# Kernel optimization log

Hardware: AMD Instinct MI355X
Metric: run time of the kernel (lower is better)

## Reference

```python
import jax, jax.numpy as jnp
import numpy as np

EMBED_DIM = 1024
NUM_HEADS = 16
HEAD_DIM = EMBED_DIM // NUM_HEADS
L, B, S = 2048, 2, 2048


def setup_inputs() -> dict:
    key = jax.random.key(0)
    k1, k2, k3, k4, k5, k6, k7 = jax.random.split(key, 7)
    query = jax.random.normal(k1, (L, B, EMBED_DIM), dtype=jnp.float32)
    kk = jax.random.normal(k2, (S, B, EMBED_DIM), dtype=jnp.float32)
    vv = jax.random.normal(k3, (S, B, EMBED_DIM), dtype=jnp.float32)
    # in_proj: Linear(E, 3E) -> weight (3E, E), bias (3E,)
    w_in = jax.random.normal(k4, (3 * EMBED_DIM, EMBED_DIM), dtype=jnp.float32) * (1.0 / np.sqrt(EMBED_DIM))
    b_in = jax.random.normal(k5, (3 * EMBED_DIM,), dtype=jnp.float32) * 0.02
    w_out = jax.random.normal(k6, (EMBED_DIM, EMBED_DIM), dtype=jnp.float32) * (1.0 / np.sqrt(EMBED_DIM))
    b_out = jax.random.normal(k7, (EMBED_DIM,), dtype=jnp.float32) * 0.02
    return {"query": query, "key": kk, "value": vv,
            "w_in": w_in, "b_in": b_in, "w_out": w_out, "b_out": b_out}


def _split_heads(x, seq_len, batch):
    # (T, B, E) -> (B, H, T, d)
    return x.reshape(seq_len, batch, NUM_HEADS, HEAD_DIM).transpose(1, 2, 0, 3)


def reference(query, key, value, w_in, b_in, w_out, b_out):
    seq_q, batch, _ = query.shape
    seq_kv = key.shape[0]
    # split fused in_proj into q/k/v projections (chunk along output rows)
    wq, wk, wv = jnp.split(w_in, 3, axis=0)
    bq, bk, bv = jnp.split(b_in, 3, axis=0)
    q = query @ wq.T + bq            # (L, B, E)
    k = key @ wk.T + bk              # (S, B, E)
    v = value @ wv.T + bv            # (S, B, E)
    q = _split_heads(q, seq_q, batch)   # (B, H, L, d)
    k = _split_heads(k, seq_kv, batch)  # (B, H, S, d)
    v = _split_heads(v, seq_kv, batch)  # (B, H, S, d)
    scale = jnp.asarray(np.sqrt(HEAD_DIM), dtype=q.dtype)
    scores = jnp.einsum('bhld,bhsd->bhls', q, k) / scale  # (B, H, L, S)
    attn = jax.nn.softmax(scores, axis=-1)
    context = jnp.einsum('bhls,bhsd->bhld', attn, v)      # (B, H, L, d)
    # (B, H, L, d) -> (L, B, E)
    context = context.transpose(2, 0, 1, 3).reshape(seq_q, batch, EMBED_DIM)
    attn_output = context @ w_out.T + b_out
    return attn_output
```

## Files before the change

### kernel.cpp

```cpp
#include <hip/hip_runtime.h>
#include <hip/hip_bf16.h>
#include <stdint.h>

#define L_SEQ 2048
#define S_SEQ 2048
#define BATCH 2
#define EMB 1024
#define NH 16
#define HD 64
#define MROWS 4096

typedef __bf16 bf16x8 __attribute__((ext_vector_type(8)));
typedef float f32x4 __attribute__((ext_vector_type(4)));
typedef __hip_bfloat16 bf16;

__device__ __forceinline__ f32x4 mfma16(bf16x8 a, bf16x8 b, f32x4 c) {
    return __builtin_amdgcn_mfma_f32_16x16x32_bf16(a, b, c, 0, 0, 0);
}

__device__ __forceinline__ void gll16(const bf16* g, bf16* l) {
    __builtin_amdgcn_global_load_lds(
        (const __attribute__((address_space(1))) void*)g,
        (__attribute__((address_space(3))) void*)l, 16, 0, 0);
}

__device__ __forceinline__ bf16x8 ld8_cvt(const float* p) {
    const float4 a = *reinterpret_cast<const float4*>(p);
    const float4 b = *reinterpret_cast<const float4*>(p + 4);
    union { bf16x8 v; bf16 h[8]; } u;
    u.h[0] = __float2bfloat16(a.x); u.h[1] = __float2bfloat16(a.y);
    u.h[2] = __float2bfloat16(a.z); u.h[3] = __float2bfloat16(a.w);
    u.h[4] = __float2bfloat16(b.x); u.h[5] = __float2bfloat16(b.y);
    u.h[6] = __float2bfloat16(b.z); u.h[7] = __float2bfloat16(b.w);
    return u.v;
}

__device__ __forceinline__ uint32_t packbf2(float a, float b) {
    union { bf16 h[2]; uint32_t u; } t;
    t.h[0] = __float2bfloat16(a); t.h[1] = __float2bfloat16(b);
    return t.u;
}

__global__ __launch_bounds__(256) void cvt_kernel(
    const float* __restrict__ w_in, const float* __restrict__ w_out,
    const float* __restrict__ q_in, const float* __restrict__ k_in,
    const float* __restrict__ v_in,
    bf16* __restrict__ wib, bf16* __restrict__ wob,
    bf16* __restrict__ Xq, bf16* __restrict__ Xk, bf16* __restrict__ Xv)
{
    const size_t i = ((size_t)blockIdx.x * 256 + threadIdx.x) * 8;
    const size_t o1 = (size_t)3 * EMB * EMB;
    const size_t o2 = o1 + (size_t)EMB * EMB;
    const size_t o3 = o2 + (size_t)MROWS * EMB;
    const size_t o4 = o3 + (size_t)MROWS * EMB;
    const float* src; bf16* dst; size_t j;
    if      (i < o1) { src = w_in;  dst = wib; j = i; }
    else if (i < o2) { src = w_out; dst = wob; j = i - o1; }
    else if (i < o3) { src = q_in;  dst = Xq;  j = i - o2; }
    else if (i < o4) { src = k_in;  dst = Xk;  j = i - o3; }
    else             { src = v_in;  dst = Xv;  j = i - o4; }
    *reinterpret_cast<bf16x8*>(dst + j) = ld8_cvt(src + j);
}

__global__ __launch_bounds__(256) void qkv_gemm(
    const bf16* __restrict__ Xq, const bf16* __restrict__ Xk,
    const bf16* __restrict__ Xv, const bf16* __restrict__ wib,
    const float* __restrict__ b_in,
    bf16* __restrict__ Qh, bf16* __restrict__ Kh, bf16* __restrict__ Vh)
{
    __shared__ alignas(16) bf16 lds_a[128 * 32];
    __shared__ alignas(16) bf16 lds_b[128 * 32];

    const int tid  = threadIdx.x;
    const int lane = tid & 63;
    const int wv   = tid >> 6;
    const int quad = lane >> 4;
    const int lx   = lane & 15;

    const int m0  = blockIdx.x * 128;
    const int n0g = blockIdx.y * 128;
    const int chunk = n0g >> 10;
    const bf16* Aop = (chunk == 0) ? Xq : (chunk == 1) ? Xk : Xv;

    const int wm = (wv >> 1) * 64;
    const int wn = (wv & 1) * 64;

    const int gr = 16 * wv + (lane >> 2);
    const int gc = (lane & 3) * 8;
    const bf16* gA = Aop + (size_t)(m0 + gr) * EMB + gc;
    const bf16* gB = wib + (size_t)(n0g + gr) * EMB + gc;
    bf16* lA = lds_a + wv * 512;
    bf16* lB = lds_b + wv * 512;

    f32x4 acc[4][4];
#pragma unroll
    for (int i = 0; i < 4; i++)
#pragma unroll
        for (int j = 0; j < 4; j++) acc[i][j] = (f32x4){0.f, 0.f, 0.f, 0.f};

    for (int kt = 0; kt < EMB; kt += 32) {
        __syncthreads();
        gll16(gA + kt, lA);
        gll16(gA + 64 * EMB + kt, lA + 2048);
        gll16(gB + kt, lB);
        gll16(gB + 64 * EMB + kt, lB + 2048);
        __syncthreads();

        bf16x8 af[4], bfv[4];
        const int ka = quad * 8;
#pragma unroll
        for (int sm = 0; sm < 4; sm++)
            af[sm] = *reinterpret_cast<const bf16x8*>(lds_a + (wm + sm * 16 + lx) * 32 + ka);
#pragma unroll
        for (int sn = 0; sn < 4; sn++)
            bfv[sn] = *reinterpret_cast<const bf16x8*>(lds_b + (wn + sn * 16 + lx) * 32 + ka);
#pragma unroll
        for (int sm = 0; sm < 4; sm++)
#pragma unroll
            for (int sn = 0; sn < 4; sn++)
                acc[sm][sn] = mfma16(af[sm], bfv[sn], acc[sm][sn]);
    }

    const float scale = (chunk == 0) ? 0.125f : 1.0f;
    bf16* dst = (chunk == 0) ? Qh : (chunk == 1) ? Kh : Vh;
#pragma unroll
    for (int sn = 0; sn < 4; sn++) {
        const int n_g = n0g + wn + sn * 16 + lx;
        const float bias = b_in[n_g];
        const int nc = n_g & (EMB - 1);
        const int h  = nc >> 6;
        const int dd = nc & 63;
#pragma unroll
        for (int sm = 0; sm < 4; sm++) {
#pragma unroll
            for (int r = 0; r < 4; r++) {
                const int m_g = m0 + wm + sm * 16 + quad * 4 + r;
                const int t = m_g >> 1;
                const int b = m_g & 1;
                const int bhidx = b * NH + h;
                const float v = (acc[sm][sn][r] + bias) * scale;
                dst[((size_t)bhidx * S_SEQ + t) * HD + dd] = __float2bfloat16(v);
            }
        }
    }
}

#define TST 72
__global__ __launch_bounds__(256) void transpose_v(
    const bf16* __restrict__ Vh, bf16* __restrict__ Vt)
{
    __shared__ alignas(16) bf16 t[64 * TST];
    const int tid = threadIdx.x;
    const int bh  = blockIdx.y;
    const int s0  = blockIdx.x * 64;
    const int r0  = tid >> 3;
    const int c0  = (tid & 7) * 8;

    const bf16* src = Vh + (size_t)bh * S_SEQ * HD;
    uint4 a = *reinterpret_cast<const uint4*>(src + (size_t)(s0 + r0) * HD + c0);
    uint4 b = *reinterpret_cast<const uint4*>(src + (size_t)(s0 + r0 + 32) * HD + c0);
    *reinterpret_cast<uint4*>(t + r0 * TST + c0) = a;
    *reinterpret_cast<uint4*>(t + (r0 + 32) * TST + c0) = b;
    __syncthreads();

    const int sc = (tid & 7) * 8;
    bf16* dst = Vt + (size_t)bh * HD * S_SEQ;
#pragma unroll
    for (int half = 0; half < 2; half++) {
        const int d = (tid >> 3) + half * 32;
        union { bf16 h[8]; uint4 u; } o;
#pragma unroll
        for (int j = 0; j < 8; j++) o.h[j] = t[(sc + j) * TST + d];
        *reinterpret_cast<uint4*>(dst + (size_t)d * S_SEQ + s0 + sc) = o.u;
    }
}

__global__ __launch_bounds__(512, 4) void attn_kernel(
    const bf16* __restrict__ Qh, const bf16* __restrict__ Kh,
    const bf16* __restrict__ Vt, bf16* __restrict__ ctx)
{
    __shared__ alignas(16) bf16 k_lds[128 * 64];
    __shared__ alignas(16) bf16 v_lds[64 * 128];
    __shared__ alignas(16) bf16 p_lds[8][16 * 128];

    const int tid  = threadIdx.x;
    const int lane = tid & 63;
    const int wv   = tid >> 6;
    const int quad = lane >> 4;
    const int lx   = lane & 15;
    const int lx7  = lane & 7;

    const int bh = blockIdx.y;
    const int l0 = blockIdx.x * 128;
    const int q0 = wv * 16;

    const bf16* Kbase = Kh + (size_t)bh * S_SEQ * HD;
    const bf16* Vbase = Vt + (size_t)bh * HD * S_SEQ;

    const bf16* qrow = Qh + ((size_t)bh * L_SEQ + l0 + q0 + lx) * HD + quad * 8;
    const bf16x8 qf0 = *reinterpret_cast<const bf16x8*>(qrow);
    const bf16x8 qf1 = *reinterpret_cast<const bf16x8*>(qrow + 32);

    float m_run = -1e30f, l_run = 0.f;
    f32x4 accv[4];
#pragma unroll
    for (int sn = 0; sn < 4; sn++) accv[sn] = (f32x4){0.f, 0.f, 0.f, 0.f};

    const int kr0 = tid >> 3;
    const int kc  = (tid & 7) * 8;
    const int vd0 = tid >> 4;
    const int vs  = (tid & 15) * 8;

    bf16* p_w = &p_lds[wv][0];

    for (int s0 = 0; s0 < S_SEQ; s0 += 128) {
        uint4 ka = *reinterpret_cast<const uint4*>(Kbase + (size_t)(s0 + kr0) * HD + kc);
        uint4 kb = *reinterpret_cast<const uint4*>(Kbase + (size_t)(s0 + kr0 + 64) * HD + kc);
        uint4 va = *reinterpret_cast<const uint4*>(Vbase + (size_t)vd0 * S_SEQ + s0 + vs);
        uint4 vb = *reinterpret_cast<const uint4*>(Vbase + (size_t)(vd0 + 32) * S_SEQ + s0 + vs);
        __syncthreads();
        {
            const int ksw = (((kc >> 3) ^ (kr0 & 7)) << 3);
            *reinterpret_cast<uint4*>(k_lds + kr0 * 64 + ksw) = ka;
            *reinterpret_cast<uint4*>(k_lds + (kr0 + 64) * 64 + ksw) = kb;
            const int vsw = (((vs >> 3) ^ (vd0 & 7)) << 3);
            *reinterpret_cast<uint4*>(v_lds + vd0 * 128 + vsw) = va;
            *reinterpret_cast<uint4*>(v_lds + (vd0 + 32) * 128 + vsw) = vb;
        }
        __syncthreads();

        f32x4 sc[8];
#pragma unroll
        for (int c = 0; c < 8; c++) {
            const bf16* kr = k_lds + (c * 16 + lx) * 64;
            bf16x8 kf0 = *reinterpret_cast<const bf16x8*>(kr + ((quad ^ lx7) << 3));
            bf16x8 kf1 = *reinterpret_cast<const bf16x8*>(kr + (((quad + 4) ^ lx7) << 3));
            f32x4 tt = (f32x4){0.f, 0.f, 0.f, 0.f};
            tt = mfma16(kf0, qf0, tt);
            tt = mfma16(kf1, qf1, tt);
            sc[c] = tt;
        }

        float mloc = sc[0][0];
#pragma unroll
        for (int c = 0; c < 8; c++)
#pragma unroll
            for (int r = 0; r < 4; r++) mloc = fmaxf(mloc, sc[c][r]);
        mloc = fmaxf(mloc, __shfl_xor(mloc, 16));
        mloc = fmaxf(mloc, __shfl_xor(mloc, 32));
        const float mnew = fmaxf(m_run, mloc);
        const float al = __expf(m_run - mnew);
        m_run = mnew;
        float rsum = 0.f;
#pragma unroll
        for (int c = 0; c < 8; c++)
#pragma unroll
            for (int r = 0; r < 4; r++) {
                const float p = __expf(sc[c][r] - mnew);
                sc[c][r] = p;
                rsum += p;
            }
        rsum += __shfl_xor(rsum, 16);
        rsum += __shfl_xor(rsum, 32);
        l_run = l_run * al + rsum;

#pragma unroll
        for (int r = 0; r < 4; r++) {
            const float ar = __shfl(al, quad * 20 + r);
#pragma unroll
            for (int sn = 0; sn < 4; sn++) accv[sn][r] *= ar;
        }

#pragma unroll
        for (int c = 0; c < 8; c++) {
            uint2 pk;
            pk.x = packbf2(sc[c][0], sc[c][1]);
            pk.y = packbf2(sc[c][2], sc[c][3]);
            const int off = lx * 128 + ((((c * 2 + (quad >> 1)) ^ lx7)) << 3) + ((quad & 1) << 2);
            *reinterpret_cast<uint2*>(p_w + off) = pk;
        }

#pragma unroll
        for (int sk = 0; sk < 4; sk++) {
            bf16x8 pf = *reinterpret_cast<const bf16x8*>(
                p_w + lx * 128 + ((((sk * 4 + quad) ^ lx7)) << 3));
#pragma unroll
            for (int sn = 0; sn < 4; sn++) {
                const bf16* vr = v_lds + (sn * 16 + lx) * 128 + ((((sk * 4 + quad) ^ lx7)) << 3);
                accv[sn] = mfma16(pf, *reinterpret_cast<const bf16x8*>(vr), accv[sn]);
            }
        }
    }

    const int b = bh >> 4;
    const int h = bh & 15;
#pragma unroll
    for (int r = 0; r < 4; r++) {
        const float lr = __shfl(l_run, quad * 20 + r);
        const float inv = 1.f / lr;
        const int l = l0 + q0 + quad * 4 + r;
#pragma unroll
        for (int sn = 0; sn < 4; sn++) {
            const int dd = sn * 16 + lx;
            ctx[(size_t)(l * BATCH + b) * EMB + h * HD + dd] =
                __float2bfloat16(accv[sn][r] * inv);
        }
    }
}

__global__ __launch_bounds__(256) void out_gemm(
    const bf16* __restrict__ ctx, const bf16* __restrict__ wob,
    const float* __restrict__ b_out, float* __restrict__ out)
{
    __shared__ alignas(16) bf16 lds_a[128 * 32];
    __shared__ alignas(16) bf16 lds_b[128 * 32];

    const int tid  = threadIdx.x;
    const int lane = tid & 63;
    const int wv   = tid >> 6;
    const int quad = lane >> 4;
    const int lx   = lane & 15;

    const int m0 = blockIdx.x * 128;
    const int n0 = blockIdx.y * 128;

    const int wm = (wv >> 1) * 64;
    const int wn = (wv & 1) * 64;

    const int gr = 16 * wv + (lane >> 2);
    const int gc = (lane & 3) * 8;
    const bf16* gA = ctx + (size_t)(m0 + gr) * EMB + gc;
    const bf16* gB = wob + (size_t)(n0 + gr) * EMB + gc;
    bf16* lA = lds_a + wv * 512;
    bf16* lB = lds_b + wv * 512;

    f32x4 acc[4][4];
#pragma unroll
    for (int i = 0; i < 4; i++)
#pragma unroll
        for (int j = 0; j < 4; j++) acc[i][j] = (f32x4){0.f, 0.f, 0.f, 0.f};

    for (int kt = 0; kt < EMB; kt += 32) {
        __syncthreads();
        gll16(gA + kt, lA);
        gll16(gA + 64 * EMB + kt, lA + 2048);
        gll16(gB + kt, lB);
        gll16(gB + 64 * EMB + kt, lB + 2048);
        __syncthreads();

        bf16x8 af[4], bfv[4];
        const int ka = quad * 8;
#pragma unroll
        for (int sm = 0; sm < 4; sm++)
            af[sm] = *reinterpret_cast<const bf16x8*>(lds_a + (wm + sm * 16 + lx) * 32 + ka);
#pragma unroll
        for (int sn = 0; sn < 4; sn++)
            bfv[sn] = *reinterpret_cast<const bf16x8*>(lds_b + (wn + sn * 16 + lx) * 32 + ka);
#pragma unroll
        for (int sm = 0; sm < 4; sm++)
#pragma unroll
            for (int sn = 0; sn < 4; sn++)
                acc[sm][sn] = mfma16(af[sm], bfv[sn], acc[sm][sn]);
    }

#pragma unroll
    for (int sn = 0; sn < 4; sn++) {
        const int n_g = n0 + wn + sn * 16 + lx;
        const float bias = b_out[n_g];
#pragma unroll
        for (int sm = 0; sm < 4; sm++) {
#pragma unroll
            for (int r = 0; r < 4; r++) {
                const int m_g = m0 + wm + sm * 16 + quad * 4 + r;
                out[(size_t)m_g * EMB + n_g] = acc[sm][sn][r] + bias;
            }
        }
    }
}

extern "C" void kernel_launch(void* const* d_in, const int* in_sizes, int n_in,
                              void* d_out, int out_size, void* d_ws, size_t ws_size,
                              hipStream_t stream)
{
    const float* query = (const float*)d_in[0];
    const float* key_  = (const float*)d_in[1];
    const float* value = (const float*)d_in[2];
    const float* w_in  = (const float*)d_in[3];
    const float* b_in  = (const float*)d_in[4];
    const float* w_out = (const float*)d_in[5];
    const float* b_out = (const float*)d_in[6];
    float* out = (float*)d_out;

    const size_t seg = (size_t)MROWS * EMB;
    bf16* wib = (bf16*)d_ws;
    bf16* wob = wib + (size_t)3 * EMB * EMB;
    bf16* Xq  = wob + (size_t)EMB * EMB;
    bf16* Xk  = Xq + seg;
    bf16* Xv  = Xk + seg;
    bf16* Qh  = Xv + seg;
    bf16* Kh  = Qh + seg;
    bf16* Vh  = Kh + seg;
    bf16* Vt  = Xq;
    bf16* ctx = Vh;

    cvt_kernel<<<8192, 256, 0, stream>>>(w_in, w_out, query, key_, value,
                                         wib, wob, Xq, Xk, Xv);
    qkv_gemm<<<dim3(32, 24), 256, 0, stream>>>(Xq, Xk, Xv, wib, b_in, Qh, Kh, Vh);
    transpose_v<<<dim3(32, 32), 256, 0, stream>>>(Vh, Vt);
    attn_kernel<<<dim3(16, 32), 512, 0, stream>>>(Qh, Kh, Vt, ctx);
    out_gemm<<<dim3(32, 8), 256, 0, stream>>>(ctx, wob, b_out, out);
}
```

Measured before the change: 239.5 us.

## Prefetch K/V tiles, use exp2 softmax, cheaper bf16 pack, smaller out_gemm tiles

Several independent changes. The attention loop now loads the next K/V tile into registers while the current tile is being computed, so global latency overlaps with the MFMA and softmax work. The Q scale folds in log2(e) so softmax can use the hardware exp2 directly. The bf16 pack is done with integer rounding plus a byte permute. Finally, out_gemm's M tile is halved to 64 so twice as many blocks cover the GPU. The bit-trick rounding ignores NaN handling and round-to-even ties, and the prefetch wraps around to reload the first tile on the last iteration.

```diff
diff --git a/kernel.cpp b/kernel.cpp
--- a/kernel.cpp
+++ b/kernel.cpp
@@ -36,9 +36,9 @@
 }
 
 __device__ __forceinline__ uint32_t packbf2(float a, float b) {
-    union { bf16 h[2]; uint32_t u; } t;
-    t.h[0] = __float2bfloat16(a); t.h[1] = __float2bfloat16(b);
-    return t.u;
+    const uint32_t ra = __float_as_uint(a) + 0x8000u;
+    const uint32_t rb = __float_as_uint(b) + 0x8000u;
+    return __builtin_amdgcn_perm(rb, ra, 0x07060302u);
 }
 
 __global__ __launch_bounds__(256) void cvt_kernel(
@@ -121,7 +121,7 @@
                 acc[sm][sn] = mfma16(af[sm], bfv[sn], acc[sm][sn]);
     }
 
-    const float scale = (chunk == 0) ? 0.125f : 1.0f;
+    const float scale = (chunk == 0) ? 0.18033688011112042f : 1.0f;
     bf16* dst = (chunk == 0) ? Qh : (chunk == 1) ? Kh : Vh;
 #pragma unroll
     for (int sn = 0; sn < 4; sn++) {
@@ -210,24 +210,29 @@
     const int kc  = (tid & 7) * 8;
     const int vd0 = tid >> 4;
     const int vs  = (tid & 15) * 8;
+    const int ksw = (((kc >> 3) ^ (kr0 & 7)) << 3);
+    const int vsw = (((vs >> 3) ^ (vd0 & 7)) << 3);
 
     bf16* p_w = &p_lds[wv][0];
 
+    uint4 ka = *reinterpret_cast<const uint4*>(Kbase + (size_t)kr0 * HD + kc);
+    uint4 kb = *reinterpret_cast<const uint4*>(Kbase + (size_t)(kr0 + 64) * HD + kc);
+    uint4 va = *reinterpret_cast<const uint4*>(Vbase + (size_t)vd0 * S_SEQ + vs);
+    uint4 vb = *reinterpret_cast<const uint4*>(Vbase + (size_t)(vd0 + 32) * S_SEQ + vs);
+
     for (int s0 = 0; s0 < S_SEQ; s0 += 128) {
-        uint4 ka = *reinterpret_cast<const uint4*>(Kbase + (size_t)(s0 + kr0) * HD + kc);
-        uint4 kb = *reinterpret_cast<const uint4*>(Kbase + (size_t)(s0 + kr0 + 64) * HD + kc);
-        uint4 va = *reinterpret_cast<const uint4*>(Vbase + (size_t)vd0 * S_SEQ + s0 + vs);
-        uint4 vb = *reinterpret_cast<const uint4*>(Vbase + (size_t)(vd0 + 32) * S_SEQ + s0 + vs);
-        __syncthreads();
-        {
-            const int ksw = (((kc >> 3) ^ (kr0 & 7)) << 3);
-            *reinterpret_cast<uint4*>(k_lds + kr0 * 64 + ksw) = ka;
-            *reinterpret_cast<uint4*>(k_lds + (kr0 + 64) * 64 + ksw) = kb;
-            const int vsw = (((vs >> 3) ^ (vd0 & 7)) << 3);
-            *reinterpret_cast<uint4*>(v_lds + vd0 * 128 + vsw) = va;
-            *reinterpret_cast<uint4*>(v_lds + (vd0 + 32) * 128 + vsw) = vb;
-        }
-        __syncthreads();
+        __syncthreads();
+        *reinterpret_cast<uint4*>(k_lds + kr0 * 64 + ksw) = ka;
+        *reinterpret_cast<uint4*>(k_lds + (kr0 + 64) * 64 + ksw) = kb;
+        *reinterpret_cast<uint4*>(v_lds + vd0 * 128 + vsw) = va;
+        *reinterpret_cast<uint4*>(v_lds + (vd0 + 32) * 128 + vsw) = vb;
+        __syncthreads();
+
+        const int s1 = (s0 + 128) & (S_SEQ - 1);
+        ka = *reinterpret_cast<const uint4*>(Kbase + (size_t)(s1 + kr0) * HD + kc);
+        kb = *reinterpret_cast<const uint4*>(Kbase + (size_t)(s1 + kr0 + 64) * HD + kc);
+        va = *reinterpret_cast<const uint4*>(Vbase + (size_t)vd0 * S_SEQ + s1 + vs);
+        vb = *reinterpret_cast<const uint4*>(Vbase + (size_t)(vd0 + 32) * S_SEQ + s1 + vs);
 
         f32x4 sc[8];
 #pragma unroll
@@ -241,25 +246,28 @@
             sc[c] = tt;
         }
 
-        float mloc = sc[0][0];
-#pragma unroll
-        for (int c = 0; c < 8; c++)
-#pragma unroll
-            for (int r = 0; r < 4; r++) mloc = fmaxf(mloc, sc[c][r]);
+        f32x4 vm = sc[0];
+#pragma unroll
+        for (int c = 1; c < 8; c++)
+#pragma unroll
+            for (int r = 0; r < 4; r++) vm[r] = fmaxf(vm[r], sc[c][r]);
+        float mloc = fmaxf(fmaxf(vm[0], vm[1]), fmaxf(vm[2], vm[3]));
         mloc = fmaxf(mloc, __shfl_xor(mloc, 16));
         mloc = fmaxf(mloc, __shfl_xor(mloc, 32));
         const float mnew = fmaxf(m_run, mloc);
-        const float al = __expf(m_run - mnew);
+        const float al = __builtin_amdgcn_exp2f(m_run - mnew);
         m_run = mnew;
-        float rsum = 0.f;
-#pragma unroll
-        for (int c = 0; c < 8; c++)
-#pragma unroll
-            for (int r = 0; r < 4; r++) {
-                const float p = __expf(sc[c][r] - mnew);
-                sc[c][r] = p;
-                rsum += p;
-            }
+
+        const f32x4 mnew4 = (f32x4){mnew, mnew, mnew, mnew};
+        f32x4 rv = (f32x4){0.f, 0.f, 0.f, 0.f};
+#pragma unroll
+        for (int c = 0; c < 8; c++) {
+            f32x4 d = sc[c] - mnew4;
+#pragma unroll
+            for (int r = 0; r < 4; r++) sc[c][r] = __builtin_amdgcn_exp2f(d[r]);
+            rv += sc[c];
+        }
+        float rsum = (rv[0] + rv[1]) + (rv[2] + rv[3]);
         rsum += __shfl_xor(rsum, 16);
         rsum += __shfl_xor(rsum, 32);
         l_run = l_run * al + rsum;
@@ -267,6 +275,8 @@
 #pragma unroll
         for (int r = 0; r < 4; r++) {
             const float ar = __shfl(al, quad * 20 + r);
+            const f32x4 ar4 = (f32x4){ar, ar, ar, ar};
+            (void)ar4;
 #pragma unroll
             for (int sn = 0; sn < 4; sn++) accv[sn][r] *= ar;
         }
@@ -312,7 +322,7 @@
     const bf16* __restrict__ ctx, const bf16* __restrict__ wob,
     const float* __restrict__ b_out, float* __restrict__ out)
 {
-    __shared__ alignas(16) bf16 lds_a[128 * 32];
+    __shared__ alignas(16) bf16 lds_a[64 * 32];
     __shared__ alignas(16) bf16 lds_b[128 * 32];
 
     const int tid  = threadIdx.x;
@@ -321,10 +331,10 @@
     const int quad = lane >> 4;
     const int lx   = lane & 15;
 
-    const int m0 = blockIdx.x * 128;
+    const int m0 = blockIdx.x * 64;
     const int n0 = blockIdx.y * 128;
 
-    const int wm = (wv >> 1) * 64;
+    const int wm = (wv >> 1) * 32;
     const int wn = (wv & 1) * 64;
 
     const int gr = 16 * wv + (lane >> 2);
@@ -334,30 +344,29 @@
     bf16* lA = lds_a + wv * 512;
     bf16* lB = lds_b + wv * 512;
 
-    f32x4 acc[4][4];
-#pragma unroll
-    for (int i = 0; i < 4; i++)
+    f32x4 acc[2][4];
+#pragma unroll
+    for (int i = 0; i < 2; i++)
 #pragma unroll
         for (int j = 0; j < 4; j++) acc[i][j] = (f32x4){0.f, 0.f, 0.f, 0.f};
 
     for (int kt = 0; kt < EMB; kt += 32) {
         __syncthreads();
         gll16(gA + kt, lA);
-        gll16(gA + 64 * EMB + kt, lA + 2048);
         gll16(gB + kt, lB);
         gll16(gB + 64 * EMB + kt, lB + 2048);
         __syncthreads();
 
-        bf16x8 af[4], bfv[4];
+        bf16x8 af[2], bfv[4];
         const int ka = quad * 8;
 #pragma unroll
-        for (int sm = 0; sm < 4; sm++)
+        for (int sm = 0; sm < 2; sm++)
             af[sm] = *reinterpret_cast<const bf16x8*>(lds_a + (wm + sm * 16 + lx) * 32 + ka);
 #pragma unroll
         for (int sn = 0; sn < 4; sn++)
             bfv[sn] = *reinterpret_cast<const bf16x8*>(lds_b + (wn + sn * 16 + lx) * 32 + ka);
 #pragma unroll
-        for (int sm = 0; sm < 4; sm++)
+        for (int sm = 0; sm < 2; sm++)
 #pragma unroll
             for (int sn = 0; sn < 4; sn++)
                 acc[sm][sn] = mfma16(af[sm], bfv[sn], acc[sm][sn]);
@@ -368,7 +377,7 @@
         const int n_g = n0 + wn + sn * 16 + lx;
         const float bias = b_out[n_g];
 #pragma unroll
-        for (int sm = 0; sm < 4; sm++) {
+        for (int sm = 0; sm < 2; sm++) {
 #pragma unroll
             for (int r = 0; r < 4; r++) {
                 const int m_g = m0 + wm + sm * 16 + quad * 4 + r;
@@ -408,5 +417,5 @@
     qkv_gemm<<<dim3(32, 24), 256, 0, stream>>>(Xq, Xk, Xv, wib, b_in, Qh, Kh, Vh);
     transpose_v<<<dim3(32, 32), 256, 0, stream>>>(Vh, Vt);
     attn_kernel<<<dim3(16, 32), 512, 0, stream>>>(Qh, Kh, Vt, ctx);
-    out_gemm<<<dim3(32, 8), 256, 0, stream>>>(ctx, wob, b_out, out);
-}
+    out_gemm<<<dim3(64, 8), 256, 0, stream>>>(ctx, wob, b_out, out);
+}
```

Measured after the change: 238.6 us. About the same (-0.4%).
